# Optimization experiments

Hardware: AMD Instinct MI355X
Metric: run time of the kernel (lower is better)

The kernel has to match this reference:

```python
import jax, jax.numpy as jnp
import numpy as np

NUM_HEADS = 8

def setup_inputs() -> dict:
    key = jax.random.key(0)
    ks = jax.random.split(key, 7)
    B, C, H, W = 8, 256, 32, 32
    scale = 1.0 / np.sqrt(C)
    return {
        "x": jax.random.normal(ks[0], (B, C, H, W), dtype=jnp.float32),
        "Wq": jax.random.normal(ks[1], (C, C), dtype=jnp.float32) * scale,
        "bq": jax.random.normal(ks[2], (C,), dtype=jnp.float32) * 0.01,
        "Wk": jax.random.normal(ks[3], (C, C), dtype=jnp.float32) * scale,
        "bk": jax.random.normal(ks[4], (C,), dtype=jnp.float32) * 0.01,
        "Wv": jax.random.normal(ks[5], (C, C), dtype=jnp.float32) * scale,
        "bv": jax.random.normal(ks[6], (C,), dtype=jnp.float32) * 0.01,
        "gamma": jnp.zeros((1,), dtype=jnp.float32),
    }

def reference(x, Wq, bq, Wk, bk, Wv, bv, gamma):
    B, C, H, W = x.shape
    nh = NUM_HEADS
    hd = C // nh
    N = H * W
    xf = x.reshape(B, C, N)  # flatten spatial dims; 1x1 conv == channel matmul

    def proj(Wt, bt):
        y = jnp.einsum('oc,bcn->bon', Wt, xf) + bt[None, :, None]
        return y.reshape(B, nh, hd, N)

    q = proj(Wq, bq)  # [B, h, d, N]
    k = proj(Wk, bk)
    v = proj(Wv, bv)

    # scores: q^T k over head_dim -> [B, h, N, N]
    scores = jnp.einsum('bhdn,bhdm->bhnm', q, k) / (hd ** 0.5)
    attn = jax.nn.softmax(scores, axis=-1)
    # out = attn @ v^T, arranged back to [B, h, d, N]
    out = jnp.einsum('bhnm,bhdm->bhdn', attn, v).reshape(B, C, H, W)
    return gamma * out + x
```

## Files before the change

kernel.cpp:

```cpp
#include <hip/hip_runtime.h>

typedef float f4 __attribute__((ext_vector_type(4)));
typedef __bf16 bf16x8 __attribute__((ext_vector_type(8)));
typedef unsigned short us4 __attribute__((ext_vector_type(4)));
typedef unsigned short us8 __attribute__((ext_vector_type(8)));
typedef unsigned int u2 __attribute__((ext_vector_type(2)));

#define NB 8
#define NC 256
#define NSP 1024
#define NH 8
#define HD 32
#define QSCALE_L2E 0.25506065038580317f

__device__ __forceinline__ unsigned short f2bf(float f) {
  unsigned u = __builtin_bit_cast(unsigned, f);
  u += 0x7FFFu + ((u >> 16) & 1u);
  return (unsigned short)(u >> 16);
}

__device__ __forceinline__ unsigned pkbf(float a, float b) {
  unsigned r;
  asm("v_cvt_pk_bf16_f32 %0, %1, %2" : "=v"(r) : "v"(a), "v"(b));
  return r;
}

__global__ __launch_bounds__(256) void prep_kernel(
    const float* __restrict__ x, const float* __restrict__ Wq,
    const float* __restrict__ Wk, const float* __restrict__ Wv,
    unsigned short* __restrict__ xT, unsigned short* __restrict__ wbf) {
  const int t = threadIdx.x;
  if (blockIdx.z == 8) {
    const int flat = (blockIdx.y * 16 + blockIdx.x) * 256 + t;
    const float* Ws[3] = {Wq, Wk, Wv};
#pragma unroll
    for (int p = 0; p < 3; ++p) {
      const f4 v = reinterpret_cast<const f4*>(Ws[p])[flat];
      us4 o;
#pragma unroll
      for (int j = 0; j < 4; ++j) o[j] = f2bf(v[j]);
      reinterpret_cast<us4*>(wbf + (size_t)p * 65536)[flat] = o;
    }
    return;
  }
  const int b = blockIdx.z;
  const int nt = blockIdx.x * 64, ct = blockIdx.y * 64;
  __shared__ float xs[64][72];
  const int cl = t >> 4, nl = (t & 15) * 4;
#pragma unroll
  for (int r = 0; r < 4; ++r) {
    const f4 v = *reinterpret_cast<const f4*>(
        &x[((size_t)(b * NC + ct + cl + r * 16)) * NSP + nt + nl]);
    *reinterpret_cast<f4*>(&xs[cl + r * 16][nl]) = v;
  }
  __syncthreads();
  const int n = t >> 2, cq = (t & 3) * 16;
  us8 o0, o1;
#pragma unroll
  for (int i = 0; i < 8; ++i) o0[i] = f2bf(xs[cq + i][n]);
#pragma unroll
  for (int i = 0; i < 8; ++i) o1[i] = f2bf(xs[cq + 8 + i][n]);
  const size_t base = ((size_t)(b * NSP + nt + n)) * NC + ct + cq;
  *reinterpret_cast<us8*>(&xT[base]) = o0;
  *reinterpret_cast<us8*>(&xT[base + 8]) = o1;
}

template <int VMODE>
__global__ __launch_bounds__(256) void proj_kernel(
    const unsigned short* __restrict__ wbf, const float* __restrict__ bq,
    const float* __restrict__ bk, const unsigned short* __restrict__ xT,
    unsigned short* __restrict__ dq, unsigned short* __restrict__ dk) {
  const int ntile = blockIdx.x * 32;
  const int b = blockIdx.y;
  const int z = blockIdx.z;
  const unsigned short* W = wbf + (size_t)z * 65536;
  const float* bias = z ? bk : bq;
  unsigned short* dst = z ? dk : dq;
  const float scale = (VMODE || z) ? 1.0f : QSCALE_L2E;

  const int t = threadIdx.x, wid = t >> 6, lane = t & 63;
  const int lr = lane & 15, lg = lane >> 4;
  const int o0 = wid * 64;
  const size_t xbase = ((size_t)b * NSP + ntile) * NC;

  f4 acc[4][4] = {};
  for (int kk = 0; kk < NC; kk += 32) {
    bf16x8 wf[4], xf[2];
#pragma unroll
    for (int i = 0; i < 4; ++i)
      wf[i] = *reinterpret_cast<const bf16x8*>(
          &W[(size_t)(o0 + i * 16 + lr) * NC + kk + lg * 8]);
#pragma unroll
    for (int j = 0; j < 2; ++j)
      xf[j] = *reinterpret_cast<const bf16x8*>(
          &xT[xbase + (size_t)(j * 16 + lr) * NC + kk + lg * 8]);
    if (!VMODE) {
#pragma unroll
      for (int i = 0; i < 4; ++i)
#pragma unroll
        for (int j = 0; j < 2; ++j)
          acc[i][j] = __builtin_amdgcn_mfma_f32_16x16x32_bf16(wf[i], xf[j],
                                                              acc[i][j], 0, 0, 0);
    } else {
#pragma unroll
      for (int i = 0; i < 2; ++i)
#pragma unroll
        for (int j = 0; j < 4; ++j)
          acc[i][j] = __builtin_amdgcn_mfma_f32_16x16x32_bf16(xf[i], wf[j],
                                                              acc[i][j], 0, 0, 0);
    }
  }

  if (!VMODE) {
#pragma unroll
    for (int i = 0; i < 4; ++i) {
      const int o = o0 + i * 16 + lg * 4;
      const f4 bv = *reinterpret_cast<const f4*>(&bias[o]);
      const int h = o >> 5, d = o & 31;
#pragma unroll
      for (int j = 0; j < 2; ++j) {
        const int n = ntile + j * 16 + lr;
        us4 pk;
#pragma unroll
        for (int r = 0; r < 4; ++r) pk[r] = f2bf((acc[i][j][r] + bv[r]) * scale);
        *reinterpret_cast<us4*>(
            &dst[(((size_t)b * NH + h) * NSP + n) * HD + d]) = pk;
      }
    }
  } else {
#pragma unroll
    for (int j = 0; j < 4; ++j) {
      const int o = o0 + j * 16 + lr;
      const float bo = bias[o];
      const int h = o >> 5, d = o & 31;
#pragma unroll
      for (int i = 0; i < 2; ++i) {
        const int n = ntile + i * 16 + lg * 4;
        us4 pk;
#pragma unroll
        for (int r = 0; r < 4; ++r) pk[r] = f2bf(acc[i][j][r] + bo);
        *reinterpret_cast<us4*>(
            &dst[(((size_t)b * NH + h) * HD + d) * NSP + n]) = pk;
      }
    }
  }
}

__global__ __launch_bounds__(256) void attn_kernel(
    const unsigned short* __restrict__ qs, const unsigned short* __restrict__ ks,
    const unsigned short* __restrict__ vt, const float* __restrict__ x,
    const float* __restrict__ gamma, float* __restrict__ out) {
  const int t = threadIdx.x, wid = t >> 6, lane = t & 63;
  const int lr = lane & 15, lg = lane >> 4;
  const int bh = blockIdx.y;
  const int qbase = blockIdx.x * 128 + wid * 32;

  __shared__ unsigned short plds[4][32][40];
  unsigned short* pw = &plds[wid][0][0];
  unsigned short* w0 = pw + lr * 40 + lg * 4;
  const unsigned short* r0 = pw + lr * 40 + lg * 8;

  const size_t kvbase = (size_t)bh * (NSP * HD);
  const bf16x8 qa0 = *reinterpret_cast<const bf16x8*>(
      &qs[kvbase + (size_t)(qbase + lr) * HD + lg * 8]);
  const bf16x8 qa1 = *reinterpret_cast<const bf16x8*>(
      &qs[kvbase + (size_t)(qbase + 16 + lr) * HD + lg * 8]);

  const unsigned short* kp = ks + kvbase;
  const unsigned short* vp = vt + kvbase;

  f4 a00 = {0.f, 0.f, 0.f, 0.f}, a01 = a00, a10 = a00, a11 = a00;
  float ls0 = 0.f, ls1 = 0.f;

  bf16x8 kb0 = *reinterpret_cast<const bf16x8*>(&kp[(size_t)lr * HD + lg * 8]);
  bf16x8 kb1 =
      *reinterpret_cast<const bf16x8*>(&kp[(size_t)(16 + lr) * HD + lg * 8]);
  bf16x8 vb0 = *reinterpret_cast<const bf16x8*>(&vp[(size_t)lr * NSP + lg * 8]);
  bf16x8 vb1 =
      *reinterpret_cast<const bf16x8*>(&vp[(size_t)(16 + lr) * NSP + lg * 8]);

  for (int kt = 0; kt < NSP; kt += 32) {
    const bf16x8 ck0 = kb0, ck1 = kb1, cv0 = vb0, cv1 = vb1;
    const int nk = (kt + 32) & (NSP - 1);
    kb0 = *reinterpret_cast<const bf16x8*>(&kp[(size_t)(nk + lr) * HD + lg * 8]);
    kb1 = *reinterpret_cast<const bf16x8*>(
        &kp[(size_t)(nk + 16 + lr) * HD + lg * 8]);
    vb0 = *reinterpret_cast<const bf16x8*>(&vp[(size_t)lr * NSP + nk + lg * 8]);
    vb1 = *reinterpret_cast<const bf16x8*>(
        &vp[(size_t)(16 + lr) * NSP + nk + lg * 8]);

    const f4 z = {0.f, 0.f, 0.f, 0.f};
    f4 s00 = __builtin_amdgcn_mfma_f32_16x16x32_bf16(ck0, qa0, z, 0, 0, 0);
    f4 s01 = __builtin_amdgcn_mfma_f32_16x16x32_bf16(ck1, qa0, z, 0, 0, 0);
    f4 s10 = __builtin_amdgcn_mfma_f32_16x16x32_bf16(ck0, qa1, z, 0, 0, 0);
    f4 s11 = __builtin_amdgcn_mfma_f32_16x16x32_bf16(ck1, qa1, z, 0, 0, 0);

    f4 e00, e01, e10, e11;
#pragma unroll
    for (int r = 0; r < 4; ++r) {
      e00[r] = __builtin_exp2f(s00[r]);
      e01[r] = __builtin_exp2f(s01[r]);
      e10[r] = __builtin_exp2f(s10[r]);
      e11[r] = __builtin_exp2f(s11[r]);
    }
    ls0 += ((e00[0] + e00[1]) + (e00[2] + e00[3])) +
           ((e01[0] + e01[1]) + (e01[2] + e01[3]));
    ls1 += ((e10[0] + e10[1]) + (e10[2] + e10[3])) +
           ((e11[0] + e11[1]) + (e11[2] + e11[3]));

    u2 w01_0 = {pkbf(e00[0], e00[1]), pkbf(e00[2], e00[3])};
    u2 w23_0 = {pkbf(e01[0], e01[1]), pkbf(e01[2], e01[3])};
    u2 w01_1 = {pkbf(e10[0], e10[1]), pkbf(e10[2], e10[3])};
    u2 w23_1 = {pkbf(e11[0], e11[1]), pkbf(e11[2], e11[3])};
    *reinterpret_cast<u2*>(w0) = w01_0;
    *reinterpret_cast<u2*>(w0 + 16) = w23_0;
    *reinterpret_cast<u2*>(w0 + 640) = w01_1;
    *reinterpret_cast<u2*>(w0 + 656) = w23_1;

    const bf16x8 pa0 = *reinterpret_cast<const bf16x8*>(r0);
    const bf16x8 pa1 = *reinterpret_cast<const bf16x8*>(r0 + 640);

    a00 = __builtin_amdgcn_mfma_f32_16x16x32_bf16(pa0, cv0, a00, 0, 0, 0);
    a01 = __builtin_amdgcn_mfma_f32_16x16x32_bf16(pa0, cv1, a01, 0, 0, 0);
    a10 = __builtin_amdgcn_mfma_f32_16x16x32_bf16(pa1, cv0, a10, 0, 0, 0);
    a11 = __builtin_amdgcn_mfma_f32_16x16x32_bf16(pa1, cv1, a11, 0, 0, 0);
  }

  ls0 += __shfl_xor(ls0, 16);
  ls0 += __shfl_xor(ls0, 32);
  ls1 += __shfl_xor(ls1, 16);
  ls1 += __shfl_xor(ls1, 32);

  f4 li0, li1;
#pragma unroll
  for (int r = 0; r < 4; ++r) {
    const int src = (lg * 4 + r) * 4;
    li0[r] = __builtin_amdgcn_rcpf(__builtin_bit_cast(
        float, __builtin_amdgcn_ds_bpermute(src, __builtin_bit_cast(int, ls0))));
    li1[r] = __builtin_amdgcn_rcpf(__builtin_bit_cast(
        float, __builtin_amdgcn_ds_bpermute(src, __builtin_bit_cast(int, ls1))));
  }

  const int b = bh >> 3, h = bh & 7;
  const float g = gamma[0];
  const size_t ob = ((size_t)b * NC + h * HD) * NSP;

  {
    const size_t o00 = ob + (size_t)lr * NSP + qbase + lg * 4;
    const f4 xr = *reinterpret_cast<const f4*>(&x[o00]);
    f4 ov;
#pragma unroll
    for (int r = 0; r < 4; ++r) ov[r] = g * a00[r] * li0[r] + xr[r];
    *reinterpret_cast<f4*>(&out[o00]) = ov;
  }
  {
    const size_t o01 = ob + (size_t)(16 + lr) * NSP + qbase + lg * 4;
    const f4 xr = *reinterpret_cast<const f4*>(&x[o01]);
    f4 ov;
#pragma unroll
    for (int r = 0; r < 4; ++r) ov[r] = g * a01[r] * li0[r] + xr[r];
    *reinterpret_cast<f4*>(&out[o01]) = ov;
  }
  {
    const size_t o10 = ob + (size_t)lr * NSP + qbase + 16 + lg * 4;
    const f4 xr = *reinterpret_cast<const f4*>(&x[o10]);
    f4 ov;
#pragma unroll
    for (int r = 0; r < 4; ++r) ov[r] = g * a10[r] * li1[r] + xr[r];
    *reinterpret_cast<f4*>(&out[o10]) = ov;
  }
  {
    const size_t o11 = ob + (size_t)(16 + lr) * NSP + qbase + 16 + lg * 4;
    const f4 xr = *reinterpret_cast<const f4*>(&x[o11]);
    f4 ov;
#pragma unroll
    for (int r = 0; r < 4; ++r) ov[r] = g * a11[r] * li1[r] + xr[r];
    *reinterpret_cast<f4*>(&out[o11]) = ov;
  }
}

extern "C" void kernel_launch(void* const* d_in, const int* in_sizes, int n_in,
                              void* d_out, int out_size, void* d_ws,
                              size_t ws_size, hipStream_t stream) {
  const float* x = (const float*)d_in[0];
  const float* Wq = (const float*)d_in[1];
  const float* bq = (const float*)d_in[2];
  const float* Wk = (const float*)d_in[3];
  const float* bk = (const float*)d_in[4];
  const float* Wv = (const float*)d_in[5];
  const float* bv = (const float*)d_in[6];
  const float* gamma = (const float*)d_in[7];
  float* out = (float*)d_out;

  unsigned short* qs = (unsigned short*)d_ws;
  unsigned short* ks = qs + (size_t)2097152;
  unsigned short* vt = ks + (size_t)2097152;
  unsigned short* wbf = vt + (size_t)2097152;
  unsigned short* xT = wbf + (size_t)3 * 65536;

  prep_kernel<<<dim3(16, 4, 9), 256, 0, stream>>>(x, Wq, Wk, Wv, xT, wbf);
  proj_kernel<0><<<dim3(32, 8, 2), 256, 0, stream>>>(wbf, bq, bk, xT, qs, ks);
  proj_kernel<1><<<dim3(32, 8, 1), 256, 0, stream>>>(wbf + 2 * 65536, bv, bv,
                                                     xT, vt, vt);
  attn_kernel<<<dim3(8, 64), 256, 0, stream>>>(qs, ks, vt, x, gamma, out);
}
```

Before: 124.0 us.

## Merge QKV projections into one kernel, widen tiles, remap blocks per XCD

Combines the separate Q/K and V projection launches into a single kernel and widens each projection tile from 32 to 64 spatial positions, so each weight fragment load feeds twice as many MFMAs. The attention kernel now processes 64 keys per iteration instead of 32, with a wider LDS buffer for P, which halves loop overhead and gives more MFMA work between global loads. Both kernels use a 1D grid with explicit XCD-aware block mapping so blocks sharing the same batch-head K/V land on the same XCD for L2 reuse. In exchange, register use per thread rises and the projection launch has fewer blocks.

Measured after the change: 126.8 us. 1.02x slower.

```diff
diff --git a/kernel.cpp b/kernel.cpp
--- a/kernel.cpp
+++ b/kernel.cpp
@@ -65,18 +65,21 @@
   *reinterpret_cast<us8*>(&xT[base + 8]) = o1;
 }
 
-template <int VMODE>
-__global__ __launch_bounds__(256) void proj_kernel(
+__global__ __launch_bounds__(256) void proj_qkv_kernel(
     const unsigned short* __restrict__ wbf, const float* __restrict__ bq,
-    const float* __restrict__ bk, const unsigned short* __restrict__ xT,
-    unsigned short* __restrict__ dq, unsigned short* __restrict__ dk) {
-  const int ntile = blockIdx.x * 32;
-  const int b = blockIdx.y;
-  const int z = blockIdx.z;
+    const float* __restrict__ bk, const float* __restrict__ bv,
+    const unsigned short* __restrict__ xT, unsigned short* __restrict__ dq,
+    unsigned short* __restrict__ dk, unsigned short* __restrict__ dv) {
+  const int id = blockIdx.x;
+  const int xcd = id & 7, rem = id >> 3;
+  const int z = rem % 3;
+  const int p = xcd + 8 * (rem / 3);
+  const int ntile = (p & 15) * 64;
+  const int b = p >> 4;
+
   const unsigned short* W = wbf + (size_t)z * 65536;
-  const float* bias = z ? bk : bq;
-  unsigned short* dst = z ? dk : dq;
-  const float scale = (VMODE || z) ? 1.0f : QSCALE_L2E;
+  const float* bias = (z == 0) ? bq : (z == 1) ? bk : bv;
+  unsigned short* dst = (z == 0) ? dq : (z == 1) ? dk : dv;
 
   const int t = threadIdx.x, wid = t >> 6, lane = t & 63;
   const int lr = lane & 15, lg = lane >> 4;
@@ -85,44 +88,45 @@
 
   f4 acc[4][4] = {};
   for (int kk = 0; kk < NC; kk += 32) {
-    bf16x8 wf[4], xf[2];
+    bf16x8 wf[4], xf[4];
 #pragma unroll
     for (int i = 0; i < 4; ++i)
       wf[i] = *reinterpret_cast<const bf16x8*>(
           &W[(size_t)(o0 + i * 16 + lr) * NC + kk + lg * 8]);
 #pragma unroll
-    for (int j = 0; j < 2; ++j)
+    for (int j = 0; j < 4; ++j)
       xf[j] = *reinterpret_cast<const bf16x8*>(
           &xT[xbase + (size_t)(j * 16 + lr) * NC + kk + lg * 8]);
-    if (!VMODE) {
+    if (z != 2) {
 #pragma unroll
       for (int i = 0; i < 4; ++i)
 #pragma unroll
-        for (int j = 0; j < 2; ++j)
-          acc[i][j] = __builtin_amdgcn_mfma_f32_16x16x32_bf16(wf[i], xf[j],
-                                                              acc[i][j], 0, 0, 0);
+        for (int j = 0; j < 4; ++j)
+          acc[i][j] = __builtin_amdgcn_mfma_f32_16x16x32_bf16(
+              wf[i], xf[j], acc[i][j], 0, 0, 0);
     } else {
 #pragma unroll
-      for (int i = 0; i < 2; ++i)
+      for (int i = 0; i < 4; ++i)
 #pragma unroll
         for (int j = 0; j < 4; ++j)
-          acc[i][j] = __builtin_amdgcn_mfma_f32_16x16x32_bf16(xf[i], wf[j],
-                                                              acc[i][j], 0, 0, 0);
-    }
-  }
-
-  if (!VMODE) {
+          acc[i][j] = __builtin_amdgcn_mfma_f32_16x16x32_bf16(
+              xf[i], wf[j], acc[i][j], 0, 0, 0);
+    }
+  }
+
+  if (z != 2) {
+    const float scale = (z == 0) ? QSCALE_L2E : 1.0f;
 #pragma unroll
     for (int i = 0; i < 4; ++i) {
       const int o = o0 + i * 16 + lg * 4;
-      const f4 bv = *reinterpret_cast<const f4*>(&bias[o]);
+      const f4 bvv = *reinterpret_cast<const f4*>(&bias[o]);
       const int h = o >> 5, d = o & 31;
 #pragma unroll
-      for (int j = 0; j < 2; ++j) {
+      for (int j = 0; j < 4; ++j) {
         const int n = ntile + j * 16 + lr;
         us4 pk;
 #pragma unroll
-        for (int r = 0; r < 4; ++r) pk[r] = f2bf((acc[i][j][r] + bv[r]) * scale);
+        for (int r = 0; r < 4; ++r) pk[r] = f2bf((acc[i][j][r] + bvv[r]) * scale);
         *reinterpret_cast<us4*>(
             &dst[(((size_t)b * NH + h) * NSP + n) * HD + d]) = pk;
       }
@@ -134,7 +138,7 @@
       const float bo = bias[o];
       const int h = o >> 5, d = o & 31;
 #pragma unroll
-      for (int i = 0; i < 2; ++i) {
+      for (int i = 0; i < 4; ++i) {
         const int n = ntile + i * 16 + lg * 4;
         us4 pk;
 #pragma unroll
@@ -150,132 +154,130 @@
     const unsigned short* __restrict__ qs, const unsigned short* __restrict__ ks,
     const unsigned short* __restrict__ vt, const float* __restrict__ x,
     const float* __restrict__ gamma, float* __restrict__ out) {
+  const int id = blockIdx.x;
+  const int xcd = id & 7, slot = id >> 3;
+  const int bh = xcd * 8 + (slot & 7);
+  const int qt = slot >> 3;
   const int t = threadIdx.x, wid = t >> 6, lane = t & 63;
   const int lr = lane & 15, lg = lane >> 4;
-  const int bh = blockIdx.y;
-  const int qbase = blockIdx.x * 128 + wid * 32;
-
-  __shared__ unsigned short plds[4][32][40];
+  const int qbase = qt * 128 + wid * 32;
+
+  __shared__ unsigned short plds[4][32][72];
   unsigned short* pw = &plds[wid][0][0];
-  unsigned short* w0 = pw + lr * 40 + lg * 4;
-  const unsigned short* r0 = pw + lr * 40 + lg * 8;
 
   const size_t kvbase = (size_t)bh * (NSP * HD);
-  const bf16x8 qa0 = *reinterpret_cast<const bf16x8*>(
-      &qs[kvbase + (size_t)(qbase + lr) * HD + lg * 8]);
-  const bf16x8 qa1 = *reinterpret_cast<const bf16x8*>(
-      &qs[kvbase + (size_t)(qbase + 16 + lr) * HD + lg * 8]);
+  bf16x8 qa[2];
+#pragma unroll
+  for (int qf = 0; qf < 2; ++qf)
+    qa[qf] = *reinterpret_cast<const bf16x8*>(
+        &qs[kvbase + (size_t)(qbase + qf * 16 + lr) * HD + lg * 8]);
 
   const unsigned short* kp = ks + kvbase;
   const unsigned short* vp = vt + kvbase;
 
-  f4 a00 = {0.f, 0.f, 0.f, 0.f}, a01 = a00, a10 = a00, a11 = a00;
-  float ls0 = 0.f, ls1 = 0.f;
-
-  bf16x8 kb0 = *reinterpret_cast<const bf16x8*>(&kp[(size_t)lr * HD + lg * 8]);
-  bf16x8 kb1 =
-      *reinterpret_cast<const bf16x8*>(&kp[(size_t)(16 + lr) * HD + lg * 8]);
-  bf16x8 vb0 = *reinterpret_cast<const bf16x8*>(&vp[(size_t)lr * NSP + lg * 8]);
-  bf16x8 vb1 =
-      *reinterpret_cast<const bf16x8*>(&vp[(size_t)(16 + lr) * NSP + lg * 8]);
-
-  for (int kt = 0; kt < NSP; kt += 32) {
-    const bf16x8 ck0 = kb0, ck1 = kb1, cv0 = vb0, cv1 = vb1;
-    const int nk = (kt + 32) & (NSP - 1);
-    kb0 = *reinterpret_cast<const bf16x8*>(&kp[(size_t)(nk + lr) * HD + lg * 8]);
-    kb1 = *reinterpret_cast<const bf16x8*>(
-        &kp[(size_t)(nk + 16 + lr) * HD + lg * 8]);
-    vb0 = *reinterpret_cast<const bf16x8*>(&vp[(size_t)lr * NSP + nk + lg * 8]);
-    vb1 = *reinterpret_cast<const bf16x8*>(
-        &vp[(size_t)(16 + lr) * NSP + nk + lg * 8]);
-
-    const f4 z = {0.f, 0.f, 0.f, 0.f};
-    f4 s00 = __builtin_amdgcn_mfma_f32_16x16x32_bf16(ck0, qa0, z, 0, 0, 0);
-    f4 s01 = __builtin_amdgcn_mfma_f32_16x16x32_bf16(ck1, qa0, z, 0, 0, 0);
-    f4 s10 = __builtin_amdgcn_mfma_f32_16x16x32_bf16(ck0, qa1, z, 0, 0, 0);
-    f4 s11 = __builtin_amdgcn_mfma_f32_16x16x32_bf16(ck1, qa1, z, 0, 0, 0);
-
-    f4 e00, e01, e10, e11;
-#pragma unroll
-    for (int r = 0; r < 4; ++r) {
-      e00[r] = __builtin_exp2f(s00[r]);
-      e01[r] = __builtin_exp2f(s01[r]);
-      e10[r] = __builtin_exp2f(s10[r]);
-      e11[r] = __builtin_exp2f(s11[r]);
-    }
-    ls0 += ((e00[0] + e00[1]) + (e00[2] + e00[3])) +
-           ((e01[0] + e01[1]) + (e01[2] + e01[3]));
-    ls1 += ((e10[0] + e10[1]) + (e10[2] + e10[3])) +
-           ((e11[0] + e11[1]) + (e11[2] + e11[3]));
-
-    u2 w01_0 = {pkbf(e00[0], e00[1]), pkbf(e00[2], e00[3])};
-    u2 w23_0 = {pkbf(e01[0], e01[1]), pkbf(e01[2], e01[3])};
-    u2 w01_1 = {pkbf(e10[0], e10[1]), pkbf(e10[2], e10[3])};
-    u2 w23_1 = {pkbf(e11[0], e11[1]), pkbf(e11[2], e11[3])};
-    *reinterpret_cast<u2*>(w0) = w01_0;
-    *reinterpret_cast<u2*>(w0 + 16) = w23_0;
-    *reinterpret_cast<u2*>(w0 + 640) = w01_1;
-    *reinterpret_cast<u2*>(w0 + 656) = w23_1;
-
-    const bf16x8 pa0 = *reinterpret_cast<const bf16x8*>(r0);
-    const bf16x8 pa1 = *reinterpret_cast<const bf16x8*>(r0 + 640);
-
-    a00 = __builtin_amdgcn_mfma_f32_16x16x32_bf16(pa0, cv0, a00, 0, 0, 0);
-    a01 = __builtin_amdgcn_mfma_f32_16x16x32_bf16(pa0, cv1, a01, 0, 0, 0);
-    a10 = __builtin_amdgcn_mfma_f32_16x16x32_bf16(pa1, cv0, a10, 0, 0, 0);
-    a11 = __builtin_amdgcn_mfma_f32_16x16x32_bf16(pa1, cv1, a11, 0, 0, 0);
-  }
-
-  ls0 += __shfl_xor(ls0, 16);
-  ls0 += __shfl_xor(ls0, 32);
-  ls1 += __shfl_xor(ls1, 16);
-  ls1 += __shfl_xor(ls1, 32);
-
-  f4 li0, li1;
-#pragma unroll
-  for (int r = 0; r < 4; ++r) {
-    const int src = (lg * 4 + r) * 4;
-    li0[r] = __builtin_amdgcn_rcpf(__builtin_bit_cast(
-        float, __builtin_amdgcn_ds_bpermute(src, __builtin_bit_cast(int, ls0))));
-    li1[r] = __builtin_amdgcn_rcpf(__builtin_bit_cast(
-        float, __builtin_amdgcn_ds_bpermute(src, __builtin_bit_cast(int, ls1))));
+  f4 acc[2][2] = {};
+  float ls[2] = {0.f, 0.f};
+
+  bf16x8 kb[4], vb[4];
+#pragma unroll
+  for (int kf = 0; kf < 4; ++kf)
+    kb[kf] = *reinterpret_cast<const bf16x8*>(
+        &kp[(size_t)(kf * 16 + lr) * HD + lg * 8]);
+#pragma unroll
+  for (int i = 0; i < 4; ++i) {
+    const int sk = i >> 1, c = i & 1;
+    vb[i] = *reinterpret_cast<const bf16x8*>(
+        &vp[(size_t)(c * 16 + lr) * NSP + sk * 32 + lg * 8]);
+  }
+
+  for (int kt = 0; kt < NSP; kt += 64) {
+    bf16x8 ck[4], cv[4];
+#pragma unroll
+    for (int i = 0; i < 4; ++i) { ck[i] = kb[i]; cv[i] = vb[i]; }
+    const int nk = (kt + 64) & (NSP - 1);
+#pragma unroll
+    for (int kf = 0; kf < 4; ++kf)
+      kb[kf] = *reinterpret_cast<const bf16x8*>(
+          &kp[(size_t)(nk + kf * 16 + lr) * HD + lg * 8]);
+#pragma unroll
+    for (int i = 0; i < 4; ++i) {
+      const int sk = i >> 1, c = i & 1;
+      vb[i] = *reinterpret_cast<const bf16x8*>(
+          &vp[(size_t)(c * 16 + lr) * NSP + nk + sk * 32 + lg * 8]);
+    }
+
+    const f4 z4 = {0.f, 0.f, 0.f, 0.f};
+    f4 st[2][4];
+#pragma unroll
+    for (int qf = 0; qf < 2; ++qf)
+#pragma unroll
+      for (int kf = 0; kf < 4; ++kf)
+        st[qf][kf] =
+            __builtin_amdgcn_mfma_f32_16x16x32_bf16(ck[kf], qa[qf], z4, 0, 0, 0);
+
+#pragma unroll
+    for (int qf = 0; qf < 2; ++qf) {
+      float lsum = 0.f;
+#pragma unroll
+      for (int kf = 0; kf < 4; ++kf) {
+        f4 e;
+#pragma unroll
+        for (int r = 0; r < 4; ++r) e[r] = __builtin_exp2f(st[qf][kf][r]);
+        lsum += (e[0] + e[1]) + (e[2] + e[3]);
+        u2 wv = {pkbf(e[0], e[1]), pkbf(e[2], e[3])};
+        *reinterpret_cast<u2*>(&pw[(qf * 16 + lr) * 72 + kf * 16 + lg * 4]) = wv;
+      }
+      ls[qf] += lsum;
+    }
+
+    bf16x8 pa[2][2];
+#pragma unroll
+    for (int sk = 0; sk < 2; ++sk)
+#pragma unroll
+      for (int qf = 0; qf < 2; ++qf)
+        pa[sk][qf] = *reinterpret_cast<const bf16x8*>(
+            &pw[(qf * 16 + lr) * 72 + sk * 32 + lg * 8]);
+
+#pragma unroll
+    for (int sk = 0; sk < 2; ++sk)
+#pragma unroll
+      for (int qf = 0; qf < 2; ++qf)
+#pragma unroll
+        for (int c = 0; c < 2; ++c)
+          acc[qf][c] = __builtin_amdgcn_mfma_f32_16x16x32_bf16(
+              pa[sk][qf], cv[sk * 2 + c], acc[qf][c], 0, 0, 0);
+  }
+
+#pragma unroll
+  for (int qf = 0; qf < 2; ++qf) {
+    ls[qf] += __shfl_xor(ls[qf], 16);
+    ls[qf] += __shfl_xor(ls[qf], 32);
   }
 
   const int b = bh >> 3, h = bh & 7;
   const float g = gamma[0];
   const size_t ob = ((size_t)b * NC + h * HD) * NSP;
 
-  {
-    const size_t o00 = ob + (size_t)lr * NSP + qbase + lg * 4;
-    const f4 xr = *reinterpret_cast<const f4*>(&x[o00]);
-    f4 ov;
-#pragma unroll
-    for (int r = 0; r < 4; ++r) ov[r] = g * a00[r] * li0[r] + xr[r];
-    *reinterpret_cast<f4*>(&out[o00]) = ov;
-  }
-  {
-    const size_t o01 = ob + (size_t)(16 + lr) * NSP + qbase + lg * 4;
-    const f4 xr = *reinterpret_cast<const f4*>(&x[o01]);
-    f4 ov;
-#pragma unroll
-    for (int r = 0; r < 4; ++r) ov[r] = g * a01[r] * li0[r] + xr[r];
-    *reinterpret_cast<f4*>(&out[o01]) = ov;
-  }
-  {
-    const size_t o10 = ob + (size_t)lr * NSP + qbase + 16 + lg * 4;
-    const f4 xr = *reinterpret_cast<const f4*>(&x[o10]);
-    f4 ov;
-#pragma unroll
-    for (int r = 0; r < 4; ++r) ov[r] = g * a10[r] * li1[r] + xr[r];
-    *reinterpret_cast<f4*>(&out[o10]) = ov;
-  }
-  {
-    const size_t o11 = ob + (size_t)(16 + lr) * NSP + qbase + 16 + lg * 4;
-    const f4 xr = *reinterpret_cast<const f4*>(&x[o11]);
-    f4 ov;
-#pragma unroll
-    for (int r = 0; r < 4; ++r) ov[r] = g * a11[r] * li1[r] + xr[r];
-    *reinterpret_cast<f4*>(&out[o11]) = ov;
+#pragma unroll
+  for (int qf = 0; qf < 2; ++qf) {
+    f4 li;
+#pragma unroll
+    for (int r = 0; r < 4; ++r) {
+      const int src = (lg * 4 + r) * 4;
+      li[r] = __builtin_amdgcn_rcpf(__builtin_bit_cast(
+          float,
+          __builtin_amdgcn_ds_bpermute(src, __builtin_bit_cast(int, ls[qf]))));
+    }
+#pragma unroll
+    for (int c = 0; c < 2; ++c) {
+      const size_t oa =
+          ob + (size_t)(c * 16 + lr) * NSP + qbase + qf * 16 + lg * 4;
+      const f4 xr = *reinterpret_cast<const f4*>(&x[oa]);
+      f4 ov;
+#pragma unroll
+      for (int r = 0; r < 4; ++r) ov[r] = g * acc[qf][c][r] * li[r] + xr[r];
+      *reinterpret_cast<f4*>(&out[oa]) = ov;
+    }
   }
 }
 
@@ -299,8 +301,7 @@
   unsigned short* xT = wbf + (size_t)3 * 65536;
 
   prep_kernel<<<dim3(16, 4, 9), 256, 0, stream>>>(x, Wq, Wk, Wv, xT, wbf);
-  proj_kernel<0><<<dim3(32, 8, 2), 256, 0, stream>>>(wbf, bq, bk, xT, qs, ks);
-  proj_kernel<1><<<dim3(32, 8, 1), 256, 0, stream>>>(wbf + 2 * 65536, bv, bv,
-                                                     xT, vt, vt);
-  attn_kernel<<<dim3(8, 64), 256, 0, stream>>>(qs, ks, vt, x, gamma, out);
-}
+  proj_qkv_kernel<<<dim3(384), 256, 0, stream>>>(wbf, bq, bk, bv, xT, qs, ks,
+                                                 vt);
+  attn_kernel<<<dim3(512), 256, 0, stream>>>(qs, ks, vt, x, gamma, out);
+}
```
